# Kernel optimization log

Hardware: AMD Instinct MI355X
Metric: run time of the kernel (lower is better)

## Reference

```python
import jax, jax.numpy as jnp
import numpy as np

N, N1, N2, K = 65536, 16384, 8192, 16
INDIM, HID, OUT = 64, 32, 128


def _knn_np(pos, q, k, chunk=1024):
    # brute-force chunked KNN (indices into pos) for setup only
    out = []
    for s in range(0, q.shape[0], chunk):
        d = ((q[s:s + chunk, None, :] - pos[None, :, :]) ** 2).sum(-1)
        out.append(np.argpartition(d, k, axis=1)[:, :k])
    return np.concatenate(out, 0)


def setup_inputs() -> dict:
    key = jax.random.key(0)
    ks = jax.random.split(key, 12)
    x = jax.random.normal(ks[0], (N, INDIM), jnp.float32)
    pos = jax.random.uniform(ks[1], (N, 3), jnp.float32)

    pos_np = np.asarray(pos)
    rng = np.random.default_rng(0)
    idx1 = np.sort(rng.choice(N, N1, replace=False))            # RandomSampler(ratio1)
    nn1 = _knn_np(pos_np, pos_np[idx1], K)                      # [N1, K] into full cloud
    src1, dst1 = nn1.reshape(-1), np.repeat(np.arange(N1), K)
    pos1 = pos_np[idx1]
    idx2 = np.sort(rng.choice(N1, N2, replace=False))           # RandomSampler(ratio2)
    nn2 = _knn_np(pos1, pos1[idx2], K)                          # [N2, K] into level-1 cloud
    src2, dst2 = nn2.reshape(-1), np.repeat(np.arange(N2), K)

    def lin(k, i, o):
        return jax.random.normal(k, (i, o), jnp.float32) / float(np.sqrt(i))

    return dict(
        x=x, pos=pos,
        W_down=lin(ks[2], INDIM, HID), b_down=jnp.zeros((HID,), jnp.float32),
        W_pp1=lin(ks[3], 10, 32), b_pp1=jnp.zeros((32,), jnp.float32),
        W_att1=lin(ks[4], 64, 64), b_att1=jnp.zeros((64,), jnp.float32),
        W_g1=lin(ks[5], 64, 64), b_g1=jnp.zeros((64,), jnp.float32),
        W_pp2=lin(ks[6], 10, 64), b_pp2=jnp.zeros((64,), jnp.float32),
        W_att2=lin(ks[7], 128, 128), b_att2=jnp.zeros((128,), jnp.float32),
        W_g2=lin(ks[8], 128, 128), b_g2=jnp.zeros((128,), jnp.float32),
        W_up=lin(ks[9], 128, OUT), b_up=jnp.zeros((OUT,), jnp.float32),
        W_sc=lin(ks[10], INDIM, OUT), b_sc=jnp.zeros((OUT,), jnp.float32),
        idx1=jnp.asarray(idx1, jnp.int32), idx2=jnp.asarray(idx2, jnp.int32),
        src1=jnp.asarray(src1, jnp.int32), dst1=jnp.asarray(dst1, jnp.int32),
        src2=jnp.asarray(src2, jnp.int32), dst2=jnp.asarray(dst2, jnp.int32),
    )


def _mlp(h, W, b):
    return jax.nn.relu(h @ W + b)


def _randla_conv(x, pos_all, pos_q, src, dst, Wpp, bpp, Watt, batt, Wg, bg, n_out):
    # RandlaKernel.message + add-aggregate + update (bipartite: targets = sampled points)
    pos_i, pos_j = pos_q[dst], pos_all[src]                     # [E,3]
    vij = pos_i - pos_j
    dij = jnp.sqrt((vij * vij).sum(-1, keepdims=True))          # [E,1]
    rel = jnp.concatenate([pos_i, pos_j, vij, dij], axis=1)     # [E,10]
    rij = _mlp(rel, Wpp, bpp)                                   # point_pos_nn
    fij = jnp.concatenate([x[src], rij], axis=1)                # [E, c+d]
    s = jax.nn.softmax(_mlp(fij, Watt, batt), axis=-1)          # softmax over feature dim (as in source)
    agg = jax.ops.segment_sum(s * fij, dst, num_segments=n_out) # aggr='add'
    return _mlp(agg, Wg, bg)                                    # global_nn


def reference(x, pos, W_down, b_down, W_pp1, b_pp1, W_att1, b_att1, W_g1, b_g1,
              W_pp2, b_pp2, W_att2, b_att2, W_g2, b_g2, W_up, b_up, W_sc, b_sc,
              idx1, idx2, src1, dst1, src2, dst2):
    h = _mlp(x, W_down, b_down)                                 # features_downsample (indim -> outdim//4)
    pos1 = pos[idx1]
    h = _randla_conv(h, pos, pos1, src1, dst1, W_pp1, b_pp1, W_att1, b_att1, W_g1, b_g1, N1)
    pos2 = pos1[idx2]
    h = _randla_conv(h, pos1, pos2, src2, dst2, W_pp2, b_pp2, W_att2, b_att2, W_g2, b_g2, N2)
    h = _mlp(h, W_up, b_up)                                     # features_upsample
    sc = _mlp(x[idx1][idx2], W_sc, b_sc)                        # shortcut resized, idx = idx1[idx2]
    return jax.nn.relu(h + sc)
```

## Files before the change

### kernel.cpp

```cpp
#include <hip/hip_runtime.h>

#define N_FULL 65536
#define NN1    16384
#define NN2    8192

typedef __attribute__((ext_vector_type(8))) short bf16x8;
typedef __attribute__((ext_vector_type(4))) float f32x4;
typedef unsigned short ushortT;

#define MFMA16(acc, a, b) acc = __builtin_amdgcn_mfma_f32_16x16x32_bf16(a, b, acc, 0, 0, 0)

#if __has_builtin(__builtin_amdgcn_cvt_pk_bf16_f32)
typedef __attribute__((ext_vector_type(2))) __bf16 bf16x2t;
static __device__ __forceinline__ unsigned pack2(float a, float b) {
    union { bf16x2t v; unsigned u; } c;
    c.v = __builtin_amdgcn_cvt_pk_bf16_f32(a, b);
    return c.u;
}
static __device__ __forceinline__ ushortT f2bf(float f) {
    union { bf16x2t v; ushortT s[2]; } c;
    c.v = __builtin_amdgcn_cvt_pk_bf16_f32(f, 0.f);
    return c.s[0];
}
#else
static __device__ __forceinline__ ushortT f2bf(float f) {
    union { float f; unsigned u; } v; v.f = f;
    unsigned r = v.u + 0x7FFFu + ((v.u >> 16) & 1u);
    return (ushortT)(r >> 16);
}
static __device__ __forceinline__ unsigned pack2(float a, float b) {
    return (unsigned)f2bf(a) | ((unsigned)f2bf(b) << 16);
}
#endif

static __device__ __forceinline__ float bfu2f(ushortT h) {
    union { unsigned u; float f; } v; v.u = (unsigned)h << 16; return v.f;
}

#define WS_WAT1  2304
#define WS_WGT1  6912
#define WS_WAT2  11520
#define WS_WGT2  28928
#define WS_WUPT  46336
#define WS_WSCT  63744
#define WS_H0    73728
#define WS_H1    (WS_H0 + 65536u*32u)
#define WS_AGG2  (WS_H1 + 16384u*64u)

static __device__ __forceinline__ void tpose(
    const float* __restrict__ src, ushortT* __restrict__ dst,
    int K, int N, int STR, int gid, int gs)
{
    for (int i = gid; i < K * N; i += gs) {
        const int n = i / K, k = i - n * K;
        dst[n * STR + k] = f2bf(src[(size_t)k * N + n]);
    }
}

__global__ __launch_bounds__(256) void k_down(
    const float* __restrict__ x, const float* __restrict__ Wd,
    const float* __restrict__ bd,
    const float* __restrict__ Wa1, const float* __restrict__ Wg1,
    const float* __restrict__ Wa2, const float* __restrict__ Wg2,
    const float* __restrict__ Wup, const float* __restrict__ Wsc,
    ushortT* __restrict__ wsw, ushortT* __restrict__ h0w)
{
    const int t = threadIdx.x;
    if (blockIdx.x >= 512) {
        const int gid = (blockIdx.x - 512) * 256 + t, gs = 68 * 256;
        tpose(Wa1, wsw + WS_WAT1, 64, 64, 72, gid, gs);
        tpose(Wg1, wsw + WS_WGT1, 64, 64, 72, gid, gs);
        tpose(Wa2, wsw + WS_WAT2, 128, 128, 136, gid, gs);
        tpose(Wg2, wsw + WS_WGT2, 128, 128, 136, gid, gs);
        tpose(Wup, wsw + WS_WUPT, 128, 128, 136, gid, gs);
        tpose(Wsc, wsw + WS_WSCT, 64, 128, 72, gid, gs);
        return;
    }

    __shared__ __align__(16) ushortT Al[128 * 72];
    __shared__ __align__(16) ushortT Bl[32 * 72];
    const int rowBase = blockIdx.x * 128;

    {
        const int r = t >> 1, c0 = (t & 1) * 32;
        unsigned* dst = (unsigned*)Al + r * 36 + (c0 >> 1);
        const float* src = &x[(size_t)(rowBase + r) * 64 + c0];
#pragma unroll
        for (int j = 0; j < 32; j += 4) {
            const float4 v = *reinterpret_cast<const float4*>(src + j);
            dst[(j >> 1) + 0] = pack2(v.x, v.y);
            dst[(j >> 1) + 1] = pack2(v.z, v.w);
        }
        const int n = t >> 3, kc = (t & 7) * 8;
        float v[8];
#pragma unroll
        for (int j = 0; j < 8; ++j) v[j] = Wd[(size_t)(kc + j) * 32 + n];
        uint4 p;
        p.x = pack2(v[0], v[1]); p.y = pack2(v[2], v[3]);
        p.z = pack2(v[4], v[5]); p.w = pack2(v[6], v[7]);
        *(uint4*)((unsigned*)Bl + n * 36 + (kc >> 1)) = p;
    }
    __syncthreads();

    const int lane = t & 63, w = t >> 6, quad = lane >> 4, c16 = lane & 15;
    f32x4 acc[2][2];
#pragma unroll
    for (int mt = 0; mt < 2; ++mt)
#pragma unroll
        for (int nt = 0; nt < 2; ++nt)
#pragma unroll
            for (int r = 0; r < 4; ++r) acc[mt][nt][r] = 0.f;
#pragma unroll
    for (int ks = 0; ks < 2; ++ks) {
        bf16x8 a[2], b[2];
#pragma unroll
        for (int mt = 0; mt < 2; ++mt)
            a[mt] = *(const bf16x8*)&Al[(w * 32 + mt * 16 + c16) * 72 + ks * 32 + quad * 8];
#pragma unroll
        for (int nt = 0; nt < 2; ++nt)
            b[nt] = *(const bf16x8*)&Bl[(nt * 16 + c16) * 72 + ks * 32 + quad * 8];
#pragma unroll
        for (int mt = 0; mt < 2; ++mt)
#pragma unroll
            for (int nt = 0; nt < 2; ++nt) MFMA16(acc[mt][nt], a[mt], b[nt]);
    }
#pragma unroll
    for (int nt = 0; nt < 2; ++nt) {
        const int col = nt * 16 + c16;
        const float bias = bd[col];
#pragma unroll
        for (int mt = 0; mt < 2; ++mt)
#pragma unroll
            for (int r = 0; r < 4; ++r) {
                const int row = rowBase + w * 32 + mt * 16 + quad * 4 + r;
                h0w[(size_t)row * 32 + col] = f2bf(fmaxf(acc[mt][nt][r] + bias, 0.f));
            }
    }
}

__global__ __launch_bounds__(256) void k_conv1(
    const ushortT* __restrict__ h0w, const float* __restrict__ pos,
    const int* __restrict__ idx1, const int* __restrict__ src1,
    const float* __restrict__ Wpp, const float* __restrict__ bpp,
    const ushortT* __restrict__ wsw, const float* __restrict__ batt,
    const float* __restrict__ bg, ushortT* __restrict__ h1w)
{
    __shared__ __align__(16) ushortT Fl[128 * 72];
    __shared__ __align__(16) ushortT A2ls[16 * 72];
    __shared__ float Pl[352];
    const int t = threadIdx.x;
    const int d0 = blockIdx.x * 8;

    for (int i = t; i < 352; i += 256) Pl[i] = (i < 320) ? Wpp[i] : bpp[i - 320];
    for (int i = t; i < 288; i += 256) ((unsigned*)A2ls)[288 + i] = 0;

    {
        const int e = t >> 1, half = t & 1;
        const int g = e >> 4;
        const int s = src1[(d0 + g) * 16 + (e & 15)];
        const uint4* srcp = (const uint4*)((const unsigned*)h0w + (size_t)s * 16 + half * 8);
        uint4* dstp = (uint4*)((unsigned*)Fl + e * 36 + half * 8);
        dstp[0] = srcp[0];
        dstp[1] = srcp[1];

        const int pin = idx1[d0 + g];
        const float pix = pos[pin * 3 + 0], piy = pos[pin * 3 + 1], piz = pos[pin * 3 + 2];
        const float pjx = pos[s * 3 + 0],  pjy = pos[s * 3 + 1],  pjz = pos[s * 3 + 2];
        const float vx = pix - pjx, vy = piy - pjy, vz = piz - pjz;
        const float dij = sqrtf(vx * vx + vy * vy + vz * vz);
        const float rel[10] = {pix, piy, piz, pjx, pjy, pjz, vx, vy, vz, dij};
        __syncthreads();
        const int c0 = half * 16;
#pragma unroll
        for (int c = 0; c < 16; c += 2) {
            float a0 = Pl[320 + c0 + c], a1 = Pl[320 + c0 + c + 1];
#pragma unroll
            for (int i = 0; i < 10; ++i) {
                a0 += rel[i] * Pl[i * 32 + c0 + c];
                a1 += rel[i] * Pl[i * 32 + c0 + c + 1];
            }
            ((unsigned*)Fl)[(e * 72 + 32 + c0 + c) >> 1] = pack2(fmaxf(a0, 0.f), fmaxf(a1, 0.f));
        }
    }
    __syncthreads();

    const int lane = t & 63, w = t >> 6, quad = lane >> 4, c16 = lane & 15;
    const ushortT* WB = wsw + WS_WAT1;
    f32x4 acc[2][4];
#pragma unroll
    for (int mt = 0; mt < 2; ++mt)
#pragma unroll
        for (int nt = 0; nt < 4; ++nt)
#pragma unroll
            for (int r = 0; r < 4; ++r) acc[mt][nt][r] = 0.f;
#pragma unroll
    for (int ks = 0; ks < 2; ++ks) {
        bf16x8 a[2];
#pragma unroll
        for (int mt = 0; mt < 2; ++mt)
            a[mt] = *(const bf16x8*)&Fl[(w * 32 + mt * 16 + c16) * 72 + ks * 32 + quad * 8];
#pragma unroll
        for (int nt = 0; nt < 4; ++nt) {
            const bf16x8 b = *(const bf16x8*)&WB[(nt * 16 + c16) * 72 + ks * 32 + quad * 8];
#pragma unroll
            for (int mt = 0; mt < 2; ++mt) MFMA16(acc[mt][nt], a[mt], b);
        }
    }
    float bcol[4];
#pragma unroll
    for (int nt = 0; nt < 4; ++nt) bcol[nt] = batt[nt * 16 + c16];

#pragma unroll
    for (int mt = 0; mt < 2; ++mt) {
#pragma unroll
        for (int nt = 0; nt < 4; ++nt)
#pragma unroll
            for (int r = 0; r < 4; ++r)
                acc[mt][nt][r] = fmaxf(acc[mt][nt][r] + bcol[nt], 0.f);
        float rs[4];
#pragma unroll
        for (int r = 0; r < 4; ++r) {
            float mx = acc[mt][0][r];
#pragma unroll
            for (int nt = 1; nt < 4; ++nt) mx = fmaxf(mx, acc[mt][nt][r]);
            mx = fmaxf(mx, __shfl_xor(mx, 1));
            mx = fmaxf(mx, __shfl_xor(mx, 2));
            mx = fmaxf(mx, __shfl_xor(mx, 4));
            mx = fmaxf(mx, __shfl_xor(mx, 8));
            float sm = 0.f;
#pragma unroll
            for (int nt = 0; nt < 4; ++nt) {
                acc[mt][nt][r] = __expf(acc[mt][nt][r] - mx);
                sm += acc[mt][nt][r];
            }
            sm += __shfl_xor(sm, 1);
            sm += __shfl_xor(sm, 2);
            sm += __shfl_xor(sm, 4);
            sm += __shfl_xor(sm, 8);
            rs[r] = 1.f / sm;
        }
#pragma unroll
        for (int nt = 0; nt < 4; ++nt) {
            float v = 0.f;
#pragma unroll
            for (int r = 0; r < 4; ++r) {
                const float fv = bfu2f(Fl[(w * 32 + mt * 16 + quad * 4 + r) * 72 + nt * 16 + c16]);
                v += acc[mt][nt][r] * rs[r] * fv;
            }
            v += __shfl_xor(v, 16);
            v += __shfl_xor(v, 32);
            if (lane < 16)
                A2ls[(w * 2 + mt) * 72 + nt * 16 + c16] = f2bf(v);
        }
    }
    __syncthreads();

    {
        const ushortT* GB = wsw + WS_WGT1;
        f32x4 acc2 = {0.f, 0.f, 0.f, 0.f};
#pragma unroll
        for (int ks = 0; ks < 2; ++ks) {
            const bf16x8 a = *(const bf16x8*)&A2ls[c16 * 72 + ks * 32 + quad * 8];
            const bf16x8 b = *(const bf16x8*)&GB[(w * 16 + c16) * 72 + ks * 32 + quad * 8];
            MFMA16(acc2, a, b);
        }
        const int col = w * 16 + c16;
        const float bias = bg[col];
        if (quad < 2) {
#pragma unroll
            for (int r = 0; r < 4; ++r) {
                const int row = quad * 4 + r;
                h1w[(size_t)(d0 + row) * 64 + col] = f2bf(fmaxf(acc2[r] + bias, 0.f));
            }
        }
    }
}

__global__ __launch_bounds__(256) void k_conv2(
    const ushortT* __restrict__ h1w, const float* __restrict__ pos,
    const int* __restrict__ idx1, const int* __restrict__ idx2,
    const int* __restrict__ src2,
    const float* __restrict__ Wpp, const float* __restrict__ bpp,
    const ushortT* __restrict__ wsw, const float* __restrict__ batt,
    ushortT* __restrict__ agg2w)
{
    __shared__ __align__(16) ushortT Fl[128 * 136];
    __shared__ float Pl[704];
    const int t = threadIdx.x;
    const int d0 = blockIdx.x * 8;

    for (int i = t; i < 704; i += 256) Pl[i] = (i < 640) ? Wpp[i] : bpp[i - 640];

    {
        const int e = t >> 1, half = t & 1;
        const int g = e >> 4;
        const int s = src2[(d0 + g) * 16 + (e & 15)];
        const uint4* srcp = (const uint4*)((const unsigned*)h1w + (size_t)s * 32 + half * 16);
        uint4* dstp = (uint4*)((unsigned*)Fl + e * 68 + half * 16);
#pragma unroll
        for (int j = 0; j < 4; ++j) dstp[j] = srcp[j];

        const int pin = idx1[idx2[d0 + g]];
        const int sn = idx1[s];
        const float pix = pos[pin * 3 + 0], piy = pos[pin * 3 + 1], piz = pos[pin * 3 + 2];
        const float pjx = pos[sn * 3 + 0],  pjy = pos[sn * 3 + 1],  pjz = pos[sn * 3 + 2];
        const float vx = pix - pjx, vy = piy - pjy, vz = piz - pjz;
        const float dij = sqrtf(vx * vx + vy * vy + vz * vz);
        const float rel[10] = {pix, piy, piz, pjx, pjy, pjz, vx, vy, vz, dij};
        __syncthreads();
        const int c0 = half * 32;
#pragma unroll
        for (int c = 0; c < 32; c += 2) {
            float a0 = Pl[640 + c0 + c], a1 = Pl[640 + c0 + c + 1];
#pragma unroll
            for (int i = 0; i < 10; ++i) {
                a0 += rel[i] * Pl[i * 64 + c0 + c];
                a1 += rel[i] * Pl[i * 64 + c0 + c + 1];
            }
            ((unsigned*)Fl)[(e * 136 + 64 + c0 + c) >> 1] = pack2(fmaxf(a0, 0.f), fmaxf(a1, 0.f));
        }
    }
    __syncthreads();

    const int lane = t & 63, w = t >> 6, quad = lane >> 4, c16 = lane & 15;
    const ushortT* WB = wsw + WS_WAT2;
    f32x4 acc[2][8];
#pragma unroll
    for (int mt = 0; mt < 2; ++mt)
#pragma unroll
        for (int nt = 0; nt < 8; ++nt)
#pragma unroll
            for (int r = 0; r < 4; ++r) acc[mt][nt][r] = 0.f;
#pragma unroll
    for (int ks = 0; ks < 4; ++ks) {
        bf16x8 a[2];
#pragma unroll
        for (int mt = 0; mt < 2; ++mt)
            a[mt] = *(const bf16x8*)&Fl[(w * 32 + mt * 16 + c16) * 136 + ks * 32 + quad * 8];
#pragma unroll
        for (int nt = 0; nt < 8; ++nt) {
            const bf16x8 b = *(const bf16x8*)&WB[(nt * 16 + c16) * 136 + ks * 32 + quad * 8];
#pragma unroll
            for (int mt = 0; mt < 2; ++mt) MFMA16(acc[mt][nt], a[mt], b);
        }
    }
    float bcol[8];
#pragma unroll
    for (int nt = 0; nt < 8; ++nt) bcol[nt] = batt[nt * 16 + c16];

#pragma unroll
    for (int mt = 0; mt < 2; ++mt) {
#pragma unroll
        for (int nt = 0; nt < 8; ++nt)
#pragma unroll
            for (int r = 0; r < 4; ++r)
                acc[mt][nt][r] = fmaxf(acc[mt][nt][r] + bcol[nt], 0.f);
        float rs[4];
#pragma unroll
        for (int r = 0; r < 4; ++r) {
            float mx = acc[mt][0][r];
#pragma unroll
            for (int nt = 1; nt < 8; ++nt) mx = fmaxf(mx, acc[mt][nt][r]);
            mx = fmaxf(mx, __shfl_xor(mx, 1));
            mx = fmaxf(mx, __shfl_xor(mx, 2));
            mx = fmaxf(mx, __shfl_xor(mx, 4));
            mx = fmaxf(mx, __shfl_xor(mx, 8));
            float sm = 0.f;
#pragma unroll
            for (int nt = 0; nt < 8; ++nt) {
                acc[mt][nt][r] = __expf(acc[mt][nt][r] - mx);
                sm += acc[mt][nt][r];
            }
            sm += __shfl_xor(sm, 1);
            sm += __shfl_xor(sm, 2);
            sm += __shfl_xor(sm, 4);
            sm += __shfl_xor(sm, 8);
            rs[r] = 1.f / sm;
        }
#pragma unroll
        for (int nt = 0; nt < 8; ++nt) {
            float v = 0.f;
#pragma unroll
            for (int r = 0; r < 4; ++r) {
                const float fv = bfu2f(Fl[(w * 32 + mt * 16 + quad * 4 + r) * 136 + nt * 16 + c16]);
                v += acc[mt][nt][r] * rs[r] * fv;
            }
            v += __shfl_xor(v, 16);
            v += __shfl_xor(v, 32);
            if (lane < 16)
                agg2w[(size_t)(d0 + w * 2 + mt) * 128 + nt * 16 + c16] = f2bf(v);
        }
    }
}

__global__ __launch_bounds__(256) void k_post(
    const ushortT* __restrict__ agg2w, const float* __restrict__ x,
    const int* __restrict__ idx1, const int* __restrict__ idx2,
    const ushortT* __restrict__ wsw,
    const float* __restrict__ bg, const float* __restrict__ bup,
    const float* __restrict__ bsc, float* __restrict__ out)
{
    __shared__ __align__(16) ushortT Al[32 * 136];
    __shared__ __align__(16) ushortT Bl[32 * 136];
    __shared__ __align__(16) ushortT A2[32 * 72];
    const int t = threadIdx.x;
    const int d0 = blockIdx.x * 32;

    for (int i = t; i < 512; i += 256) {
        const int r = i >> 4, j = i & 15;
        ((uint4*)((unsigned*)Al + r * 68))[j] =
            ((const uint4*)((const unsigned*)agg2w + (size_t)(d0 + r) * 64))[j];
    }
    {
        const int r = t >> 3, q = t & 7;
        const int pin = idx1[idx2[d0 + r]];
        const float* src = &x[(size_t)pin * 64 + q * 8];
        unsigned* dst = (unsigned*)A2 + r * 36 + q * 4;
#pragma unroll
        for (int j = 0; j < 4; ++j) {
            const float2 v = *reinterpret_cast<const float2*>(src + j * 2);
            dst[j] = pack2(v.x, v.y);
        }
    }
    __syncthreads();

    const int lane = t & 63, w = t >> 6, quad = lane >> 4, c16 = lane & 15;
    const int mtw = w >> 1;
    const int ntb = (w & 1) * 4;

    {
        const ushortT* WB = wsw + WS_WGT2;
        f32x4 acc[4];
#pragma unroll
        for (int nt = 0; nt < 4; ++nt)
#pragma unroll
            for (int r = 0; r < 4; ++r) acc[nt][r] = 0.f;
#pragma unroll
        for (int ks = 0; ks < 4; ++ks) {
            const bf16x8 a = *(const bf16x8*)&Al[(mtw * 16 + c16) * 136 + ks * 32 + quad * 8];
#pragma unroll
            for (int nt = 0; nt < 4; ++nt) {
                const bf16x8 b = *(const bf16x8*)&WB[((ntb + nt) * 16 + c16) * 136 + ks * 32 + quad * 8];
                MFMA16(acc[nt], a, b);
            }
        }
#pragma unroll
        for (int nt = 0; nt < 4; ++nt) {
            const int col = (ntb + nt) * 16 + c16;
            const float bias = bg[col];
#pragma unroll
            for (int r = 0; r < 4; ++r)
                Bl[(mtw * 16 + quad * 4 + r) * 136 + col] = f2bf(fmaxf(acc[nt][r] + bias, 0.f));
        }
    }
    __syncthreads();

    f32x4 u[4];
    {
        const ushortT* WB = wsw + WS_WUPT;
#pragma unroll
        for (int nt = 0; nt < 4; ++nt)
#pragma unroll
            for (int r = 0; r < 4; ++r) u[nt][r] = 0.f;
#pragma unroll
        for (int ks = 0; ks < 4; ++ks) {
            const bf16x8 a = *(const bf16x8*)&Bl[(mtw * 16 + c16) * 136 + ks * 32 + quad * 8];
#pragma unroll
            for (int nt = 0; nt < 4; ++nt) {
                const bf16x8 b = *(const bf16x8*)&WB[((ntb + nt) * 16 + c16) * 136 + ks * 32 + quad * 8];
                MFMA16(u[nt], a, b);
            }
        }
#pragma unroll
        for (int nt = 0; nt < 4; ++nt) {
            const float bias = bup[(ntb + nt) * 16 + c16];
#pragma unroll
            for (int r = 0; r < 4; ++r) u[nt][r] = fmaxf(u[nt][r] + bias, 0.f);
        }
    }

    {
        const ushortT* WB = wsw + WS_WSCT;
        f32x4 acc[4];
#pragma unroll
        for (int nt = 0; nt < 4; ++nt)
#pragma unroll
            for (int r = 0; r < 4; ++r) acc[nt][r] = 0.f;
#pragma unroll
        for (int ks = 0; ks < 2; ++ks) {
            const bf16x8 a = *(const bf16x8*)&A2[(mtw * 16 + c16) * 72 + ks * 32 + quad * 8];
#pragma unroll
            for (int nt = 0; nt < 4; ++nt) {
                const bf16x8 b = *(const bf16x8*)&WB[((ntb + nt) * 16 + c16) * 72 + ks * 32 + quad * 8];
                MFMA16(acc[nt], a, b);
            }
        }
#pragma unroll
        for (int nt = 0; nt < 4; ++nt) {
            const int col = (ntb + nt) * 16 + c16;
            const float bias = bsc[col];
#pragma unroll
            for (int r = 0; r < 4; ++r) {
                const float sc = fmaxf(acc[nt][r] + bias, 0.f);
                const int row = d0 + mtw * 16 + quad * 4 + r;
                out[(size_t)row * 128 + col] = u[nt][r] + sc;
            }
        }
    }
}

extern "C" void kernel_launch(void* const* d_in, const int* in_sizes, int n_in,
                              void* d_out, int out_size, void* d_ws, size_t ws_size,
                              hipStream_t stream)
{
    const float* x      = (const float*)d_in[0];
    const float* pos    = (const float*)d_in[1];
    const float* W_down = (const float*)d_in[2];
    const float* b_down = (const float*)d_in[3];
    const float* W_pp1  = (const float*)d_in[4];
    const float* b_pp1  = (const float*)d_in[5];
    const float* W_att1 = (const float*)d_in[6];
    const float* b_att1 = (const float*)d_in[7];
    const float* W_g1   = (const float*)d_in[8];
    const float* b_g1   = (const float*)d_in[9];
    const float* W_pp2  = (const float*)d_in[10];
    const float* b_pp2  = (const float*)d_in[11];
    const float* W_att2 = (const float*)d_in[12];
    const float* b_att2 = (const float*)d_in[13];
    const float* W_g2   = (const float*)d_in[14];
    const float* b_g2   = (const float*)d_in[15];
    const float* W_up   = (const float*)d_in[16];
    const float* b_up   = (const float*)d_in[17];
    const float* W_sc   = (const float*)d_in[18];
    const float* b_sc   = (const float*)d_in[19];
    const int* idx1 = (const int*)d_in[20];
    const int* idx2 = (const int*)d_in[21];
    const int* src1 = (const int*)d_in[22];
    const int* src2 = (const int*)d_in[24];

    ushortT* wsw = (ushortT*)d_ws;
    ushortT* h0w   = wsw + WS_H0;
    ushortT* h1w   = wsw + WS_H1;
    ushortT* agg2w = wsw + WS_AGG2;

    k_down <<<512 + 68, 256, 0, stream>>>(x, W_down, b_down,
                                          W_att1, W_g1, W_att2, W_g2, W_up, W_sc,
                                          wsw, h0w);
    k_conv1<<<NN1 / 8, 256, 0, stream>>>(h0w, pos, idx1, src1,
                                         W_pp1, b_pp1, wsw, b_att1, b_g1, h1w);
    k_conv2<<<NN2 / 8, 256, 0, stream>>>(h1w, pos, idx1, idx2, src2,
                                         W_pp2, b_pp2, wsw, b_att2, agg2w);
    k_post <<<NN2 / 32, 256, 0, stream>>>(agg2w, x, idx1, idx2, wsw,
                                          b_g2, b_up, b_sc, (float*)d_out);
}
```

Baseline: 180.5 us.

## Fuse post-MLP stages into conv2 and use fixed softmax shift

Merges the k_post kernel (global_nn, upsample and shortcut MLPs) into conv2, so the aggregated features stay in shared memory and the agg2 workspace round trip and one launch go away. Both conv kernels now skip the per-row max reduction in the softmax and subtract a fixed constant of 24 instead. Since the relu'd logits are non-negative this is safe unless a logit exceeds roughly 24+88, where exp overflows, or all logits are far below 24, where exp underflows. The fused epilogue runs with only 8 rows per block, so half the MFMA rows are wasted and the weight reads from wsw are repeated across more blocks.

```diff
diff --git a/kernel.cpp b/kernel.cpp
--- a/kernel.cpp
+++ b/kernel.cpp
@@ -45,7 +45,8 @@
 #define WS_WSCT  63744
 #define WS_H0    73728
 #define WS_H1    (WS_H0 + 65536u*32u)
-#define WS_AGG2  (WS_H1 + 16384u*64u)
+
+#define SMAX_SHIFT 24.0f
 
 static __device__ __forceinline__ void tpose(
     const float* __restrict__ src, ushortT* __restrict__ dst,
@@ -212,25 +213,14 @@
 
 #pragma unroll
     for (int mt = 0; mt < 2; ++mt) {
-#pragma unroll
-        for (int nt = 0; nt < 4; ++nt)
-#pragma unroll
-            for (int r = 0; r < 4; ++r)
-                acc[mt][nt][r] = fmaxf(acc[mt][nt][r] + bcol[nt], 0.f);
         float rs[4];
 #pragma unroll
         for (int r = 0; r < 4; ++r) {
-            float mx = acc[mt][0][r];
-#pragma unroll
-            for (int nt = 1; nt < 4; ++nt) mx = fmaxf(mx, acc[mt][nt][r]);
-            mx = fmaxf(mx, __shfl_xor(mx, 1));
-            mx = fmaxf(mx, __shfl_xor(mx, 2));
-            mx = fmaxf(mx, __shfl_xor(mx, 4));
-            mx = fmaxf(mx, __shfl_xor(mx, 8));
             float sm = 0.f;
 #pragma unroll
             for (int nt = 0; nt < 4; ++nt) {
-                acc[mt][nt][r] = __expf(acc[mt][nt][r] - mx);
+                const float a = fmaxf(acc[mt][nt][r] + bcol[nt], 0.f);
+                acc[mt][nt][r] = __expf(a - SMAX_SHIFT);
                 sm += acc[mt][nt][r];
             }
             sm += __shfl_xor(sm, 1);
@@ -276,15 +266,19 @@
     }
 }
 
-__global__ __launch_bounds__(256) void k_conv2(
+__global__ __launch_bounds__(256) void k_conv2f(
     const ushortT* __restrict__ h1w, const float* __restrict__ pos,
+    const float* __restrict__ x,
     const int* __restrict__ idx1, const int* __restrict__ idx2,
     const int* __restrict__ src2,
     const float* __restrict__ Wpp, const float* __restrict__ bpp,
     const ushortT* __restrict__ wsw, const float* __restrict__ batt,
-    ushortT* __restrict__ agg2w)
+    const float* __restrict__ bg, const float* __restrict__ bup,
+    const float* __restrict__ bsc, float* __restrict__ out)
 {
     __shared__ __align__(16) ushortT Fl[128 * 136];
+    __shared__ __align__(16) ushortT AGG[16 * 136];
+    __shared__ __align__(16) ushortT H2[16 * 136];
     __shared__ float Pl[704];
     const int t = threadIdx.x;
     const int d0 = blockIdx.x * 8;
@@ -350,25 +344,14 @@
 
 #pragma unroll
     for (int mt = 0; mt < 2; ++mt) {
-#pragma unroll
-        for (int nt = 0; nt < 8; ++nt)
-#pragma unroll
-            for (int r = 0; r < 4; ++r)
-                acc[mt][nt][r] = fmaxf(acc[mt][nt][r] + bcol[nt], 0.f);
         float rs[4];
 #pragma unroll
         for (int r = 0; r < 4; ++r) {
-            float mx = acc[mt][0][r];
-#pragma unroll
-            for (int nt = 1; nt < 8; ++nt) mx = fmaxf(mx, acc[mt][nt][r]);
-            mx = fmaxf(mx, __shfl_xor(mx, 1));
-            mx = fmaxf(mx, __shfl_xor(mx, 2));
-            mx = fmaxf(mx, __shfl_xor(mx, 4));
-            mx = fmaxf(mx, __shfl_xor(mx, 8));
             float sm = 0.f;
 #pragma unroll
             for (int nt = 0; nt < 8; ++nt) {
-                acc[mt][nt][r] = __expf(acc[mt][nt][r] - mx);
+                const float a = fmaxf(acc[mt][nt][r] + bcol[nt], 0.f);
+                acc[mt][nt][r] = __expf(a - SMAX_SHIFT);
                 sm += acc[mt][nt][r];
             }
             sm += __shfl_xor(sm, 1);
@@ -388,122 +371,96 @@
             v += __shfl_xor(v, 16);
             v += __shfl_xor(v, 32);
             if (lane < 16)
-                agg2w[(size_t)(d0 + w * 2 + mt) * 128 + nt * 16 + c16] = f2bf(v);
-        }
-    }
-}
-
-__global__ __launch_bounds__(256) void k_post(
-    const ushortT* __restrict__ agg2w, const float* __restrict__ x,
-    const int* __restrict__ idx1, const int* __restrict__ idx2,
-    const ushortT* __restrict__ wsw,
-    const float* __restrict__ bg, const float* __restrict__ bup,
-    const float* __restrict__ bsc, float* __restrict__ out)
-{
-    __shared__ __align__(16) ushortT Al[32 * 136];
-    __shared__ __align__(16) ushortT Bl[32 * 136];
-    __shared__ __align__(16) ushortT A2[32 * 72];
-    const int t = threadIdx.x;
-    const int d0 = blockIdx.x * 32;
-
-    for (int i = t; i < 512; i += 256) {
-        const int r = i >> 4, j = i & 15;
-        ((uint4*)((unsigned*)Al + r * 68))[j] =
-            ((const uint4*)((const unsigned*)agg2w + (size_t)(d0 + r) * 64))[j];
-    }
-    {
-        const int r = t >> 3, q = t & 7;
-        const int pin = idx1[idx2[d0 + r]];
-        const float* src = &x[(size_t)pin * 64 + q * 8];
-        unsigned* dst = (unsigned*)A2 + r * 36 + q * 4;
-#pragma unroll
-        for (int j = 0; j < 4; ++j) {
-            const float2 v = *reinterpret_cast<const float2*>(src + j * 2);
-            dst[j] = pack2(v.x, v.y);
+                AGG[(w * 2 + mt) * 136 + nt * 16 + c16] = f2bf(v);
         }
     }
     __syncthreads();
 
-    const int lane = t & 63, w = t >> 6, quad = lane >> 4, c16 = lane & 15;
-    const int mtw = w >> 1;
-    const int ntb = (w & 1) * 4;
-
-    {
-        const ushortT* WB = wsw + WS_WGT2;
-        f32x4 acc[4];
-#pragma unroll
-        for (int nt = 0; nt < 4; ++nt)
-#pragma unroll
-            for (int r = 0; r < 4; ++r) acc[nt][r] = 0.f;
+
+    {
+        const ushortT* GB = wsw + WS_WGT2;
+        f32x4 g[2];
+#pragma unroll
+        for (int j = 0; j < 2; ++j)
+#pragma unroll
+            for (int r = 0; r < 4; ++r) g[j][r] = 0.f;
 #pragma unroll
         for (int ks = 0; ks < 4; ++ks) {
-            const bf16x8 a = *(const bf16x8*)&Al[(mtw * 16 + c16) * 136 + ks * 32 + quad * 8];
-#pragma unroll
-            for (int nt = 0; nt < 4; ++nt) {
-                const bf16x8 b = *(const bf16x8*)&WB[((ntb + nt) * 16 + c16) * 136 + ks * 32 + quad * 8];
-                MFMA16(acc[nt], a, b);
-            }
-        }
-#pragma unroll
-        for (int nt = 0; nt < 4; ++nt) {
-            const int col = (ntb + nt) * 16 + c16;
+            const bf16x8 a = *(const bf16x8*)&AGG[c16 * 136 + ks * 32 + quad * 8];
+#pragma unroll
+            for (int j = 0; j < 2; ++j) {
+                const bf16x8 b = *(const bf16x8*)&GB[((w * 2 + j) * 16 + c16) * 136 + ks * 32 + quad * 8];
+                MFMA16(g[j], a, b);
+            }
+        }
+#pragma unroll
+        for (int j = 0; j < 2; ++j) {
+            const int col = (w * 2 + j) * 16 + c16;
             const float bias = bg[col];
 #pragma unroll
             for (int r = 0; r < 4; ++r)
-                Bl[(mtw * 16 + quad * 4 + r) * 136 + col] = f2bf(fmaxf(acc[nt][r] + bias, 0.f));
+                H2[(quad * 4 + r) * 136 + col] = f2bf(fmaxf(g[j][r] + bias, 0.f));
         }
     }
     __syncthreads();
 
-    f32x4 u[4];
-    {
-        const ushortT* WB = wsw + WS_WUPT;
-#pragma unroll
-        for (int nt = 0; nt < 4; ++nt)
-#pragma unroll
-            for (int r = 0; r < 4; ++r) u[nt][r] = 0.f;
+    f32x4 u[2];
+    {
+        const ushortT* UB = wsw + WS_WUPT;
+#pragma unroll
+        for (int j = 0; j < 2; ++j)
+#pragma unroll
+            for (int r = 0; r < 4; ++r) u[j][r] = 0.f;
 #pragma unroll
         for (int ks = 0; ks < 4; ++ks) {
-            const bf16x8 a = *(const bf16x8*)&Bl[(mtw * 16 + c16) * 136 + ks * 32 + quad * 8];
-#pragma unroll
-            for (int nt = 0; nt < 4; ++nt) {
-                const bf16x8 b = *(const bf16x8*)&WB[((ntb + nt) * 16 + c16) * 136 + ks * 32 + quad * 8];
-                MFMA16(u[nt], a, b);
-            }
-        }
-#pragma unroll
-        for (int nt = 0; nt < 4; ++nt) {
-            const float bias = bup[(ntb + nt) * 16 + c16];
-#pragma unroll
-            for (int r = 0; r < 4; ++r) u[nt][r] = fmaxf(u[nt][r] + bias, 0.f);
-        }
-    }
-
-    {
-        const ushortT* WB = wsw + WS_WSCT;
-        f32x4 acc[4];
-#pragma unroll
-        for (int nt = 0; nt < 4; ++nt)
-#pragma unroll
-            for (int r = 0; r < 4; ++r) acc[nt][r] = 0.f;
+            const bf16x8 a = *(const bf16x8*)&H2[c16 * 136 + ks * 32 + quad * 8];
+#pragma unroll
+            for (int j = 0; j < 2; ++j) {
+                const bf16x8 b = *(const bf16x8*)&UB[((w * 2 + j) * 16 + c16) * 136 + ks * 32 + quad * 8];
+                MFMA16(u[j], a, b);
+            }
+        }
+#pragma unroll
+        for (int j = 0; j < 2; ++j) {
+            const float bias = bup[(w * 2 + j) * 16 + c16];
+#pragma unroll
+            for (int r = 0; r < 4; ++r) u[j][r] = fmaxf(u[j][r] + bias, 0.f);
+        }
+    }
+
+    {
+        const ushortT* SB = wsw + WS_WSCT;
+        const int pinx = idx1[idx2[d0 + (c16 & 7)]];
+        const float* xrow = &x[(size_t)pinx * 64];
+        f32x4 s[2];
+#pragma unroll
+        for (int j = 0; j < 2; ++j)
+#pragma unroll
+            for (int r = 0; r < 4; ++r) s[j][r] = 0.f;
 #pragma unroll
         for (int ks = 0; ks < 2; ++ks) {
-            const bf16x8 a = *(const bf16x8*)&A2[(mtw * 16 + c16) * 72 + ks * 32 + quad * 8];
-#pragma unroll
-            for (int nt = 0; nt < 4; ++nt) {
-                const bf16x8 b = *(const bf16x8*)&WB[((ntb + nt) * 16 + c16) * 72 + ks * 32 + quad * 8];
-                MFMA16(acc[nt], a, b);
-            }
-        }
-#pragma unroll
-        for (int nt = 0; nt < 4; ++nt) {
-            const int col = (ntb + nt) * 16 + c16;
-            const float bias = bsc[col];
-#pragma unroll
-            for (int r = 0; r < 4; ++r) {
-                const float sc = fmaxf(acc[nt][r] + bias, 0.f);
-                const int row = d0 + mtw * 16 + quad * 4 + r;
-                out[(size_t)row * 128 + col] = u[nt][r] + sc;
+            const float4 v0 = *reinterpret_cast<const float4*>(xrow + ks * 32 + quad * 8);
+            const float4 v1 = *reinterpret_cast<const float4*>(xrow + ks * 32 + quad * 8 + 4);
+            union { bf16x8 v; unsigned u[4]; } a;
+            a.u[0] = pack2(v0.x, v0.y); a.u[1] = pack2(v0.z, v0.w);
+            a.u[2] = pack2(v1.x, v1.y); a.u[3] = pack2(v1.z, v1.w);
+#pragma unroll
+            for (int j = 0; j < 2; ++j) {
+                const bf16x8 b = *(const bf16x8*)&SB[((w * 2 + j) * 16 + c16) * 72 + ks * 32 + quad * 8];
+                MFMA16(s[j], a.v, b);
+            }
+        }
+        if (quad < 2) {
+#pragma unroll
+            for (int j = 0; j < 2; ++j) {
+                const int col = (w * 2 + j) * 16 + c16;
+                const float bias = bsc[col];
+#pragma unroll
+                for (int r = 0; r < 4; ++r) {
+                    const float sc = fmaxf(s[j][r] + bias, 0.f);
+                    const int row = d0 + quad * 4 + r;
+                    out[(size_t)row * 128 + col] = u[j][r] + sc;
+                }
             }
         }
     }
@@ -539,17 +496,15 @@
     const int* src2 = (const int*)d_in[24];
 
     ushortT* wsw = (ushortT*)d_ws;
-    ushortT* h0w   = wsw + WS_H0;
-    ushortT* h1w   = wsw + WS_H1;
-    ushortT* agg2w = wsw + WS_AGG2;
-
-    k_down <<<512 + 68, 256, 0, stream>>>(x, W_down, b_down,
-                                          W_att1, W_g1, W_att2, W_g2, W_up, W_sc,
-                                          wsw, h0w);
-    k_conv1<<<NN1 / 8, 256, 0, stream>>>(h0w, pos, idx1, src1,
-                                         W_pp1, b_pp1, wsw, b_att1, b_g1, h1w);
-    k_conv2<<<NN2 / 8, 256, 0, stream>>>(h1w, pos, idx1, idx2, src2,
-                                         W_pp2, b_pp2, wsw, b_att2, agg2w);
-    k_post <<<NN2 / 32, 256, 0, stream>>>(agg2w, x, idx1, idx2, wsw,
+    ushortT* h0w = wsw + WS_H0;
+    ushortT* h1w = wsw + WS_H1;
+
+    k_down  <<<512 + 68, 256, 0, stream>>>(x, W_down, b_down,
+                                           W_att1, W_g1, W_att2, W_g2, W_up, W_sc,
+                                           wsw, h0w);
+    k_conv1 <<<NN1 / 8, 256, 0, stream>>>(h0w, pos, idx1, src1,
+                                          W_pp1, b_pp1, wsw, b_att1, b_g1, h1w);
+    k_conv2f<<<NN2 / 8, 256, 0, stream>>>(h1w, pos, x, idx1, idx2, src2,
+                                          W_pp2, b_pp2, wsw, b_att2,
                                           b_g2, b_up, b_sc, (float*)d_out);
 }
```

Measured after the change: 177.1 us. Within noise of the previous version (-1.9%).
